# Kernel optimization log

Hardware: AMD Instinct MI355X
Metric: run time of the kernel (lower is better)

Reference implementation:

```python
import jax, jax.numpy as jnp
import numpy as np

C = 256
G = 32  # GroupNorm groups
EPS = 1e-6


def setup_inputs() -> dict:
    key = jax.random.key(0)
    ks = jax.random.split(key, 11)
    B, H, W = 4, 64, 64
    scale = 0.02
    return {
        "x": jax.random.normal(ks[0], (B, C, H, W), dtype=jnp.float32),
        "gn_scale": jnp.ones((C,), jnp.float32),
        "gn_bias": jnp.zeros((C,), jnp.float32),
        "wq": jax.random.normal(ks[1], (C, C), jnp.float32) * scale,
        "bq": jnp.zeros((C,), jnp.float32),
        "wk": jax.random.normal(ks[2], (C, C), jnp.float32) * scale,
        "bk": jnp.zeros((C,), jnp.float32),
        "wv": jax.random.normal(ks[3], (C, C), jnp.float32) * scale,
        "bv": jnp.zeros((C,), jnp.float32),
        "wp": jax.random.normal(ks[4], (C, C), jnp.float32) * scale,
        "bp": jnp.zeros((C,), jnp.float32),
    }


def _group_norm(x, scale, bias):
    b, c, h, w = x.shape
    xr = x.reshape(b, G, c // G, h, w)
    mu = jnp.mean(xr, axis=(2, 3, 4), keepdims=True)
    var = jnp.var(xr, axis=(2, 3, 4), keepdims=True)
    xn = ((xr - mu) * jax.lax.rsqrt(var + EPS)).reshape(b, c, h, w)
    return xn * scale[None, :, None, None] + bias[None, :, None, None]


def _conv1x1(x, w, bch):
    # 1x1 conv == channel-mixing matmul; w is (out_ch, in_ch)
    return jnp.einsum('bchw,dc->bdhw', x, w) + bch[None, :, None, None]


def reference(x, gn_scale, gn_bias, wq, bq, wk, bk, wv, bv, wp, bp):
    b, c, h, w = x.shape
    hn = _group_norm(x, gn_scale, gn_bias)
    q = _conv1x1(hn, wq, bq).reshape(b, c, h * w)  # (b,c,N)
    k = _conv1x1(hn, wk, bk).reshape(b, c, h * w)
    v = _conv1x1(hn, wv, bv).reshape(b, c, h * w)
    # attn[b,i,j] = softmax_j( q_i . k_j / sqrt(c) )
    attn = jax.nn.softmax(jnp.einsum('bci,bcj->bij', q, k) * (c ** -0.5), axis=-1)
    A = jnp.einsum('bcj,bij->bci', v, attn).reshape(b, c, h, w)
    return x + _conv1x1(A, wp, bp)
```

## Files before the change

kernel.cpp:

```cpp
#include <hip/hip_runtime.h>
#include <stdint.h>

#define Bn 4
#define Cn 256
#define Gn 32
#define Nn 4096
#define CGn 8

typedef unsigned short u16;
typedef __attribute__((ext_vector_type(8))) short short8;
typedef __attribute__((ext_vector_type(4))) short short4v;
typedef __attribute__((ext_vector_type(4))) float f32x4;
typedef __attribute__((ext_vector_type(16))) float f32x16;

__device__ __forceinline__ u16 f2bf(float x) {
  uint32_t u = __float_as_uint(x);
  u += 0x7fffu + ((u >> 16) & 1u);
  return (u16)(u >> 16);
}
__device__ __forceinline__ float b2f(u16 v) {
  return __uint_as_float(((uint32_t)v) << 16);
}

__device__ __forceinline__ void gl_lds16(const void* g, void* l) {
  __builtin_amdgcn_global_load_lds(
      (__attribute__((address_space(1))) void*)(uintptr_t)g,
      (__attribute__((address_space(3))) void*)(uintptr_t)l, 16, 0, 0);
}

__device__ __forceinline__ int sw512(int row, int cb) { return row * 512 + ((cb ^ (row & 7)) * 16); }

__global__ void k_cs(const float* __restrict__ wq, const float* __restrict__ wk,
                     const float* __restrict__ wv, const float* __restrict__ wp,
                     const float* __restrict__ bq, const float* __restrict__ bk,
                     const float* __restrict__ bv, const float* __restrict__ x,
                     u16* __restrict__ wqkv, u16* __restrict__ wpb,
                     float* __restrict__ bqkv, float* __restrict__ stats) {
  if (blockIdx.x < 256) {
    const float s = 0.09016844005556021f;
    int i = blockIdx.x * 256 + threadIdx.x;
    wqkv[i]          = f2bf(wq[i] * s);
    wqkv[i + 65536]  = f2bf(wk[i]);
    wqkv[i + 131072] = f2bf(wv[i]);
    wpb[i]           = f2bf(wp[i]);
    if (i < 256) { bqkv[i] = bq[i] * s; bqkv[i + 256] = bk[i]; bqkv[i + 512] = bv[i]; }
  } else {
    int blk = blockIdx.x - 256;
    int grp = blk >> 2, part = blk & 3;
    const float4* base = (const float4*)(x + (size_t)grp * (CGn * Nn) + part * 8192);
    float s = 0.f, s2 = 0.f;
    for (int i = threadIdx.x; i < 2048; i += 256) {
      float4 v = base[i];
      s  += v.x + v.y + v.z + v.w;
      s2 += v.x * v.x + v.y * v.y + v.z * v.z + v.w * v.w;
    }
#pragma unroll
    for (int m = 1; m < 64; m <<= 1) { s += __shfl_xor(s, m, 64); s2 += __shfl_xor(s2, m, 64); }
    __shared__ float ps[4], ps2[4];
    int w = threadIdx.x >> 6;
    if ((threadIdx.x & 63) == 0) { ps[w] = s; ps2[w] = s2; }
    __syncthreads();
    if (threadIdx.x == 0) {
      stats[grp * 8 + part * 2]     = ps[0] + ps[1] + ps[2] + ps[3];
      stats[grp * 8 + part * 2 + 1] = ps2[0] + ps2[1] + ps2[2] + ps2[3];
    }
  }
}

__global__ void k_apply(const float* __restrict__ x, const float* __restrict__ stats,
                        const float* __restrict__ gsc, const float* __restrict__ gbi,
                        u16* __restrict__ hnT) {
  __shared__ __align__(16) char smem[32768];
  __shared__ float smu[Gn], srs[Gn];
  int n0 = blockIdx.x * 64;
  int b = blockIdx.y;
  int tid = threadIdx.x;
  if (tid < Gn) {
    float S = 0.f, S2 = 0.f;
#pragma unroll
    for (int p = 0; p < 4; ++p) {
      S  += stats[(b * Gn + tid) * 8 + p * 2];
      S2 += stats[(b * Gn + tid) * 8 + p * 2 + 1];
    }
    const float inv = 1.f / (CGn * Nn);
    float mu = S * inv;
    float var = S2 * inv - mu * mu;
    smu[tid] = mu;
    srs[tid] = rsqrtf(var + 1e-6f);
  }
  __syncthreads();
  int nl = (tid & 15) * 4;
  int cbase = tid >> 4;
  for (int pass = 0; pass < 16; ++pass) {
    int c = pass * 16 + cbase;
    float4 v = *(const float4*)(x + (size_t)b * Cn * Nn + (size_t)c * Nn + n0 + nl);
    int g = c >> 3;
    float sc = gsc[c] * srs[g];
    float bi = gbi[c] - smu[g] * sc;
    float vals[4] = {v.x, v.y, v.z, v.w};
#pragma unroll
    for (int i = 0; i < 4; ++i) {
      int row = nl + i;
      int off = row * 512 + ((((c >> 3) + row) & 31) * 16) + (c & 7) * 2;
      *(u16*)(smem + off) = f2bf(vals[i] * sc + bi);
    }
  }
  __syncthreads();
#pragma unroll
  for (int p = 0; p < 8; ++p) {
    int idx = p * 256 + tid;
    int row = idx >> 5, pc = idx & 31;
    int gc = (pc - row) & 31;
    short8 v8 = *(const short8*)(smem + row * 512 + pc * 16);
    *(short8*)(hnT + ((size_t)b * Nn + n0 + row) * Cn + gc * 8) = v8;
  }
}

__global__ __launch_bounds__(256, 2)
void k_qkv(const u16* __restrict__ wqkv, const float* __restrict__ bqkv,
           const u16* __restrict__ hnT, u16* __restrict__ qT, u16* __restrict__ kT,
           u16* __restrict__ vv) {
  __shared__ __align__(16) char smem[65536];
  const int tid = threadIdx.x, lane = tid & 63, w = tid >> 6;
  const int quad = (lane >> 4) & 3, low = lane & 15;
  const int d0 = blockIdx.y * 64, b = blockIdx.z;
  const int n_base = blockIdx.x * 256;
  const int which = d0 >> 8;
  const int dl0 = d0 & 255;
  const u16* hb = hnT + (size_t)b * Nn * Cn;
  const int scol = lane & 31;

#define QKV_STAGE(bsel, nt)                                                     \
  {                                                                             \
    _Pragma("unroll") for (int s = 0; s < 8; ++s) {                             \
      int r = w * 16 + s * 2 + (lane >> 5);                                     \
      int gc = (scol - r) & 31;                                                 \
      gl_lds16(hb + (size_t)(n_base + (nt) * 64 + r) * Cn + gc * 8,             \
               smem + (bsel) * 32768 + (w * 16 + s * 2) * 512);                 \
    }                                                                           \
  }

  QKV_STAGE(0, 0);
  short8 af[8];
  {
    const u16* wrow = wqkv + (size_t)(d0 + w * 16 + low) * Cn + quad * 8;
#pragma unroll
    for (int kk = 0; kk < 8; ++kk) af[kk] = *(const short8*)(wrow + kk * 32);
  }
  float bias[4];
#pragma unroll
  for (int r = 0; r < 4; ++r) bias[r] = bqkv[d0 + w * 16 + quad * 4 + r];

  for (int nt = 0; nt < 4; ++nt) {
    if (nt < 3) {
      QKV_STAGE((nt + 1) & 1, nt + 1);
      asm volatile("s_waitcnt vmcnt(10)" ::: "memory");
    } else {
      asm volatile("s_waitcnt vmcnt(0)" ::: "memory");
    }
    asm volatile("s_barrier" ::: "memory");
    char* buf = smem + (nt & 1) * 32768;
    f32x4 acc[4] = {{0.f,0.f,0.f,0.f},{0.f,0.f,0.f,0.f},{0.f,0.f,0.f,0.f},{0.f,0.f,0.f,0.f}};
#pragma unroll
    for (int kk = 0; kk < 8; ++kk)
#pragma unroll
      for (int t = 0; t < 4; ++t) {
        int row = t * 16 + low;
        short8 bf = *(const short8*)(buf + row * 512 + (((kk * 4 + quad) + row) & 31) * 16);
        acc[t] = __builtin_amdgcn_mfma_f32_16x16x32_bf16(af[kk], bf, acc[t], 0, 0, 0);
      }
    asm volatile("s_barrier" ::: "memory");
    char* Q = buf + w * 8192;
    if (which == 2) {
#pragma unroll
      for (int t = 0; t < 4; ++t)
#pragma unroll
        for (int rp = 0; rp < 2; ++rp) {
          uint32_t wv2;
          float f0 = acc[t][2 * rp] + bias[2 * rp];
          float f1 = acc[t][2 * rp + 1] + bias[2 * rp + 1];
          asm("v_cvt_pk_bf16_f32 %0, %1, %2" : "=v"(wv2) : "v"(f0), "v"(f1));
          *(u16*)(Q + (quad * 4 + 2 * rp) * 144 + t * 32 + low * 2) = (u16)wv2;
          *(u16*)(Q + (quad * 4 + 2 * rp + 1) * 144 + t * 32 + low * 2) = (u16)(wv2 >> 16);
        }
#pragma unroll
      for (int s = 0; s < 2; ++s) {
        int slot = s * 64 + lane;
        int row = slot >> 3, ch = slot & 7;
        short8 v8 = *(const short8*)(Q + row * 144 + ch * 16);
        *(short8*)(vv + (size_t)b * Cn * Nn + (size_t)(dl0 + w * 16 + row) * Nn +
                   n_base + nt * 64 + ch * 8) = v8;
      }
    } else {
#pragma unroll
      for (int t = 0; t < 4; ++t) {
        union { uint32_t u[2]; short4v s; } pk;
        float f0 = acc[t][0] + bias[0], f1 = acc[t][1] + bias[1];
        float f2 = acc[t][2] + bias[2], f3 = acc[t][3] + bias[3];
        asm("v_cvt_pk_bf16_f32 %0, %1, %2" : "=v"(pk.u[0]) : "v"(f0), "v"(f1));
        asm("v_cvt_pk_bf16_f32 %0, %1, %2" : "=v"(pk.u[1]) : "v"(f2), "v"(f3));
        *(short4v*)(Q + (t * 16 + low) * 48 + quad * 8) = pk.s;
      }
      u16* dst = (which == 0 ? qT : kT) + (size_t)b * Nn * Cn;
#pragma unroll
      for (int s = 0; s < 2; ++s) {
        int slot = s * 64 + lane;
        int row = slot >> 1, half = slot & 1;
        short8 v8 = *(const short8*)(Q + row * 48 + half * 16);
        *(short8*)(dst + (size_t)(n_base + nt * 64 + row) * Cn + dl0 + w * 16 + half * 8) = v8;
      }
    }
  }
#undef QKV_STAGE
}

__device__ __forceinline__ void flash_stage(char* smem, int bsel, const u16* kTb,
                                            const u16* vb, int j0, int w, int lo,
                                            int kr, int vr, int vp) {
  char* ksb = smem + bsel * 32768;
  char* vsb = ksb + 16384;
#pragma unroll
  for (int s = 0; s < 4; ++s) {
    int j = kr + s * 2;
    int gc = (lo - j) & 31;
    gl_lds16(kTb + (size_t)(j0 + j) * Cn + gc * 8, ksb + (w * 8 + s * 2) * 512);
  }
#pragma unroll
  for (int s = 0; s < 4; ++s) {
    int c = vr + s * 16;
    int gc = (vp - c - (c >> 2)) & 3;
    gl_lds16(vb + (size_t)c * Nn + j0 + gc * 8, vsb + (w * 64 + s * 16) * 64);
  }
}

__global__ __launch_bounds__(256, 2)
void k_flash(const u16* __restrict__ qT, const u16* __restrict__ kT,
             const u16* __restrict__ vv, u16* __restrict__ Op0,
             u16* __restrict__ Op1, u16* __restrict__ Op2, u16* __restrict__ Op3,
             float* __restrict__ lrow) {
  __shared__ __align__(16) char smem[65536];
  const int tid = threadIdx.x, lane = tid & 63, w = tid >> 6;
  const int lo = lane & 31, hi = lane >> 5;
  const int i0 = blockIdx.x * 128;
  const int b = blockIdx.y, jh = blockIdx.z;
  const u16* qTb = qT + (size_t)b * Nn * Cn;
  const u16* kTb = kT + (size_t)b * Nn * Cn;
  const u16* vb  = vv + (size_t)b * Cn * Nn;
  const int u7 = lo + hi;
  const int u9 = lo + hi + (lo >> 2);
  const int kr = w * 8 + hi;
  const int vr = w * 64 + (lane >> 2);
  const int vp = lane & 3;

  flash_stage(smem, 0, kTb, vb, jh * 1024, w, lo, kr, vr, vp);

  short8 qf[16];
  {
    const u16* qrow = qTb + (size_t)(i0 + w * 32 + lo) * Cn + hi * 8;
#pragma unroll
    for (int ks = 0; ks < 16; ++ks) qf[ks] = *(const short8*)(qrow + ks * 16);
  }
  f32x16 Oa[8];
#pragma unroll
  for (int ct = 0; ct < 8; ++ct)
#pragma unroll
    for (int e = 0; e < 16; ++e) Oa[ct][e] = 0.f;
  float l_ = 0.f;

  for (int jt = 0; jt < 32; ++jt) {
    if (jt < 31) {
      flash_stage(smem, (jt + 1) & 1, kTb, vb, jh * 1024 + (jt + 1) * 32, w, lo, kr, vr, vp);
      asm volatile("s_waitcnt vmcnt(8)" ::: "memory");
    } else {
      asm volatile("s_waitcnt vmcnt(0)" ::: "memory");
    }
    asm volatile("s_barrier" ::: "memory");
    const char* ksb = smem + (jt & 1) * 32768;
    const char* vsb = ksb + 16384;

    f32x16 S0;
#pragma unroll
    for (int e = 0; e < 16; ++e) S0[e] = 0.f;
    __builtin_amdgcn_s_setprio(1);
#pragma unroll
    for (int ks = 0; ks < 16; ++ks) {
      int ch = (ks * 2 + u7) & 31;
      short8 a0 = *(const short8*)(ksb + lo * 512 + ch * 16);
      S0 = __builtin_amdgcn_mfma_f32_32x32x16_bf16(a0, qf[ks], S0, 0, 0, 0);
    }
    __builtin_amdgcn_s_setprio(0);
    uint32_t Pp[8];
#pragma unroll
    for (int g = 0; g < 8; ++g) {
      float p0 = __builtin_amdgcn_exp2f(S0[2 * g]);
      float p1 = __builtin_amdgcn_exp2f(S0[2 * g + 1]);
      l_ += p0 + p1;
      asm("v_cvt_pk_bf16_f32 %0, %1, %2" : "=v"(Pp[g]) : "v"(p0), "v"(p1));
    }
#pragma unroll
    for (int kst = 0; kst < 2; ++kst) {
      uint32_t x0 = Pp[4 * kst], x1 = Pp[4 * kst + 1];
      uint32_t y0 = Pp[4 * kst + 2], y1 = Pp[4 * kst + 3];
      asm("v_permlane32_swap_b32 %0, %1" : "+v"(x0), "+v"(y0));
      asm("v_permlane32_swap_b32 %0, %1" : "+v"(x1), "+v"(y1));
      union { uint32_t u[4]; short8 s8; } pu;
      pu.u[0] = x0;
      pu.u[1] = x1;
      pu.u[2] = y0;
      pu.u[3] = y1;
      int ch = (kst * 2 + u9) & 3;
      __builtin_amdgcn_s_setprio(1);
#pragma unroll
      for (int ct = 0; ct < 8; ++ct) {
        short8 vf = *(const short8*)(vsb + (ct * 32 + lo) * 64 + ch * 16);
        Oa[ct] = __builtin_amdgcn_mfma_f32_32x32x16_bf16(vf, pu.s8, Oa[ct], 0, 0, 0);
      }
      __builtin_amdgcn_s_setprio(0);
    }
    asm volatile("s_barrier" ::: "memory");
  }

  l_ += __shfl_xor(l_, 32, 64);
  if (hi == 0)
    lrow[(size_t)jh * (Bn * Nn) + (size_t)b * Nn + i0 + w * 32 + lo] = l_;
  float invl = __builtin_amdgcn_rcpf(l_);
  __syncthreads();
#pragma unroll
  for (int ct = 0; ct < 8; ++ct)
#pragma unroll
    for (int g = 0; g < 4; ++g) {
      union { uint32_t u[2]; short4v s; } pk;
      float f0 = Oa[ct][g * 4 + 0] * invl, f1 = Oa[ct][g * 4 + 1] * invl;
      float f2 = Oa[ct][g * 4 + 2] * invl, f3 = Oa[ct][g * 4 + 3] * invl;
      asm("v_cvt_pk_bf16_f32 %0, %1, %2" : "=v"(pk.u[0]) : "v"(f0), "v"(f1));
      asm("v_cvt_pk_bf16_f32 %0, %1, %2" : "=v"(pk.u[1]) : "v"(f2), "v"(f3));
      int chv = (ct * 4 + g + lo) & 31;
      *(short4v*)(smem + w * 16384 + lo * 512 + chv * 16 + hi * 8) = pk.s;
    }
  __syncthreads();
  u16* Opj = (jh == 0) ? Op0 : (jh == 1) ? Op1 : (jh == 2) ? Op2 : Op3;
  u16* Ob = Opj + ((size_t)b * Nn + i0 + w * 32) * (size_t)Cn;
#pragma unroll
  for (int s = 0; s < 16; ++s) {
    int rr = s * 2 + hi;
    short8 v8 = *(const short8*)(smem + w * 16384 + rr * 512 + lo * 16);
    int gc = (lo - rr) & 31;
    *(short8*)(Ob + (size_t)rr * Cn + gc * 8) = v8;
  }
}

__global__ void k_comb(const u16* __restrict__ O0, const u16* __restrict__ O1,
                       const u16* __restrict__ O2, const u16* __restrict__ O3,
                       const float* __restrict__ lrow, u16* __restrict__ OT) {
  int gid = blockIdx.x * 256 + threadIdx.x;
  int row = gid >> 6;
  int c4 = (gid & 63) << 2;
  float L = lrow[row] + lrow[Bn * Nn + row] + lrow[2 * Bn * Nn + row] + lrow[3 * Bn * Nn + row];
  float inv = __builtin_amdgcn_rcpf(L);
  size_t base = (size_t)row * Cn + c4;
  short4v a0 = *(const short4v*)(O0 + base);
  short4v a1 = *(const short4v*)(O1 + base);
  short4v a2 = *(const short4v*)(O2 + base);
  short4v a3 = *(const short4v*)(O3 + base);
  short4v o;
#pragma unroll
  for (int i = 0; i < 4; ++i)
    o[i] = (short)f2bf((b2f((u16)a0[i]) + b2f((u16)a1[i]) + b2f((u16)a2[i]) + b2f((u16)a3[i])) * inv);
  *(short4v*)(OT + base) = o;
}

__global__ __launch_bounds__(256, 2)
void k_proj(const u16* __restrict__ wpb, const float* __restrict__ bp,
            const u16* __restrict__ OT, const float* __restrict__ x,
            float* __restrict__ out) {
  __shared__ __align__(16) char smem[65536];
  int tid = threadIdx.x, lane = tid & 63, w = tid >> 6, quad = lane >> 4, low = lane & 15;
  int n0 = blockIdx.x * 64, d0 = blockIdx.y * 64, b = blockIdx.z;
  {
    int r0 = w * 16;
#pragma unroll
    for (int s = 0; s < 8; ++s) {
      int rs = r0 + s * 2;
      int r = rs + (lane >> 5);
      int cb = (lane & 31) ^ (r & 7);
      gl_lds16(wpb + (size_t)(d0 + r) * Cn + cb * 8, smem + rs * 512);
      gl_lds16(OT + ((size_t)b * Nn + n0 + r) * Cn + cb * 8, smem + 32768 + rs * 512);
    }
  }
  asm volatile("s_waitcnt vmcnt(0)" ::: "memory");
  __syncthreads();
  f32x4 acc[4] = {{0.f,0.f,0.f,0.f},{0.f,0.f,0.f,0.f},{0.f,0.f,0.f,0.f},{0.f,0.f,0.f,0.f}};
#pragma unroll
  for (int kk = 0; kk < 8; ++kk) {
    short8 af = *(const short8*)(smem + sw512(w * 16 + low, kk * 4 + quad));
#pragma unroll
    for (int t = 0; t < 4; ++t) {
      short8 bf = *(const short8*)(smem + 32768 + sw512(t * 16 + low, kk * 4 + quad));
      acc[t] = __builtin_amdgcn_mfma_f32_16x16x32_bf16(af, bf, acc[t], 0, 0, 0);
    }
  }
  int dloc = d0 + w * 16 + quad * 4;
#pragma unroll
  for (int t = 0; t < 4; ++t)
#pragma unroll
    for (int r = 0; r < 4; ++r) {
      size_t idx = (size_t)b * Cn * Nn + (size_t)(dloc + r) * Nn + n0 + t * 16 + low;
      out[idx] = x[idx] + acc[t][r] + bp[dloc + r];
    }
}

extern "C" void kernel_launch(void* const* d_in, const int* in_sizes, int n_in,
                              void* d_out, int out_size, void* d_ws, size_t ws_size,
                              hipStream_t stream) {
  const float* x   = (const float*)d_in[0];
  const float* gsc = (const float*)d_in[1];
  const float* gbi = (const float*)d_in[2];
  const float* wq  = (const float*)d_in[3];
  const float* bq  = (const float*)d_in[4];
  const float* wk  = (const float*)d_in[5];
  const float* bk  = (const float*)d_in[6];
  const float* wv  = (const float*)d_in[7];
  const float* bv  = (const float*)d_in[8];
  const float* wp  = (const float*)d_in[9];
  const float* bp  = (const float*)d_in[10];
  float* out = (float*)d_out;

  char* ws = (char*)d_ws;
  u16*   wqkv  = (u16*)(ws + 0);
  u16*   wpb   = (u16*)(ws + 393216);
  float* bqkv  = (float*)(ws + 524288);
  float* stats = (float*)(ws + 527360);
  float* lrow  = (float*)(ws + 532480);
  u16*   hnT   = (u16*)(ws + 1048576);
  u16*   qT    = (u16*)(ws + 9437184);
  u16*   kT    = (u16*)(ws + 17825792);
  u16*   vv    = (u16*)(ws + 26214400);
  u16*   Op1   = (u16*)(ws + 34603008);
  u16*   Op2   = (u16*)(ws + 42991616);
  u16*   Op3   = (u16*)(ws + 51380224);

  k_cs<<<768, 256, 0, stream>>>(wq, wk, wv, wp, bq, bk, bv, x, wqkv, wpb, bqkv, stats);
  k_apply<<<dim3(64, 4), 256, 0, stream>>>(x, stats, gsc, gbi, hnT);
  k_qkv<<<dim3(16, 12, 4), 256, 0, stream>>>(wqkv, bqkv, hnT, qT, kT, vv);
  k_flash<<<dim3(32, 4, 4), 256, 0, stream>>>(qT, kT, vv, hnT , Op1, Op2, Op3, lrow);
  k_comb<<<4096, 256, 0, stream>>>(hnT, Op1, Op2, Op3, lrow, qT );
  k_proj<<<dim3(64, 4, 4), 256, 0, stream>>>(wpb, bp, qT , x, out);
}
```

Baseline: 194.9 us.

## Fuse split-KV combine into projection kernel and split QK accumulator chain

```diff
diff --git a/kernel.cpp b/kernel.cpp
--- a/kernel.cpp
+++ b/kernel.cpp
@@ -278,22 +278,25 @@
     const char* ksb = smem + (jt & 1) * 32768;
     const char* vsb = ksb + 16384;
 
-    f32x16 S0;
-#pragma unroll
-    for (int e = 0; e < 16; ++e) S0[e] = 0.f;
+    f32x16 S0, S1;
+#pragma unroll
+    for (int e = 0; e < 16; ++e) { S0[e] = 0.f; S1[e] = 0.f; }
     __builtin_amdgcn_s_setprio(1);
 #pragma unroll
-    for (int ks = 0; ks < 16; ++ks) {
-      int ch = (ks * 2 + u7) & 31;
-      short8 a0 = *(const short8*)(ksb + lo * 512 + ch * 16);
+    for (int ks = 0; ks < 16; ks += 2) {
+      int ch0 = (ks * 2 + u7) & 31;
+      int ch1 = (ks * 2 + 2 + u7) & 31;
+      short8 a0 = *(const short8*)(ksb + lo * 512 + ch0 * 16);
+      short8 a1 = *(const short8*)(ksb + lo * 512 + ch1 * 16);
       S0 = __builtin_amdgcn_mfma_f32_32x32x16_bf16(a0, qf[ks], S0, 0, 0, 0);
+      S1 = __builtin_amdgcn_mfma_f32_32x32x16_bf16(a1, qf[ks + 1], S1, 0, 0, 0);
     }
     __builtin_amdgcn_s_setprio(0);
     uint32_t Pp[8];
 #pragma unroll
     for (int g = 0; g < 8; ++g) {
-      float p0 = __builtin_amdgcn_exp2f(S0[2 * g]);
-      float p1 = __builtin_amdgcn_exp2f(S0[2 * g + 1]);
+      float p0 = __builtin_amdgcn_exp2f(S0[2 * g] + S1[2 * g]);
+      float p1 = __builtin_amdgcn_exp2f(S0[2 * g + 1] + S1[2 * g + 1]);
       l_ += p0 + p1;
       asm("v_cvt_pk_bf16_f32 %0, %1, %2" : "=v"(Pp[g]) : "v"(p0), "v"(p1));
     }
@@ -349,30 +352,12 @@
   }
 }
 
-__global__ void k_comb(const u16* __restrict__ O0, const u16* __restrict__ O1,
-                       const u16* __restrict__ O2, const u16* __restrict__ O3,
-                       const float* __restrict__ lrow, u16* __restrict__ OT) {
-  int gid = blockIdx.x * 256 + threadIdx.x;
-  int row = gid >> 6;
-  int c4 = (gid & 63) << 2;
-  float L = lrow[row] + lrow[Bn * Nn + row] + lrow[2 * Bn * Nn + row] + lrow[3 * Bn * Nn + row];
-  float inv = __builtin_amdgcn_rcpf(L);
-  size_t base = (size_t)row * Cn + c4;
-  short4v a0 = *(const short4v*)(O0 + base);
-  short4v a1 = *(const short4v*)(O1 + base);
-  short4v a2 = *(const short4v*)(O2 + base);
-  short4v a3 = *(const short4v*)(O3 + base);
-  short4v o;
-#pragma unroll
-  for (int i = 0; i < 4; ++i)
-    o[i] = (short)f2bf((b2f((u16)a0[i]) + b2f((u16)a1[i]) + b2f((u16)a2[i]) + b2f((u16)a3[i])) * inv);
-  *(short4v*)(OT + base) = o;
-}
-
 __global__ __launch_bounds__(256, 2)
 void k_proj(const u16* __restrict__ wpb, const float* __restrict__ bp,
-            const u16* __restrict__ OT, const float* __restrict__ x,
-            float* __restrict__ out) {
+            const u16* __restrict__ O0, const u16* __restrict__ O1,
+            const u16* __restrict__ O2, const u16* __restrict__ O3,
+            const float* __restrict__ lrow,
+            const float* __restrict__ x, float* __restrict__ out) {
   __shared__ __align__(16) char smem[65536];
   int tid = threadIdx.x, lane = tid & 63, w = tid >> 6, quad = lane >> 4, low = lane & 15;
   int n0 = blockIdx.x * 64, d0 = blockIdx.y * 64, b = blockIdx.z;
@@ -384,8 +369,28 @@
       int r = rs + (lane >> 5);
       int cb = (lane & 31) ^ (r & 7);
       gl_lds16(wpb + (size_t)(d0 + r) * Cn + cb * 8, smem + rs * 512);
-      gl_lds16(OT + ((size_t)b * Nn + n0 + r) * Cn + cb * 8, smem + 32768 + rs * 512);
-    }
+    }
+  }
+#pragma unroll 4
+  for (int p = 0; p < 8; ++p) {
+    int slot = p * 256 + tid;
+    int row = slot >> 5, pc = slot & 31;
+    int gcb = pc ^ (row & 7);
+    size_t gbase = ((size_t)b * Nn + n0 + row) * Cn + gcb * 8;
+    short8 a0 = *(const short8*)(O0 + gbase);
+    short8 a1 = *(const short8*)(O1 + gbase);
+    short8 a2 = *(const short8*)(O2 + gbase);
+    short8 a3 = *(const short8*)(O3 + gbase);
+    int rrow = b * Nn + n0 + row;
+    float L = lrow[rrow] + lrow[Bn * Nn + rrow] + lrow[2 * Bn * Nn + rrow] +
+              lrow[3 * Bn * Nn + rrow];
+    float inv = __builtin_amdgcn_rcpf(L);
+    short8 o;
+#pragma unroll
+    for (int i = 0; i < 8; ++i)
+      o[i] = (short)f2bf((b2f((u16)a0[i]) + b2f((u16)a1[i]) + b2f((u16)a2[i]) +
+                          b2f((u16)a3[i])) * inv);
+    *(short8*)(smem + 32768 + row * 512 + pc * 16) = o;
   }
   asm volatile("s_waitcnt vmcnt(0)" ::: "memory");
   __syncthreads();
@@ -443,6 +448,5 @@
   k_apply<<<dim3(64, 4), 256, 0, stream>>>(x, stats, gsc, gbi, hnT);
   k_qkv<<<dim3(16, 12, 4), 256, 0, stream>>>(wqkv, bqkv, hnT, qT, kT, vv);
   k_flash<<<dim3(32, 4, 4), 256, 0, stream>>>(qT, kT, vv, hnT , Op1, Op2, Op3, lrow);
-  k_comb<<<4096, 256, 0, stream>>>(hnT, Op1, Op2, Op3, lrow, qT );
-  k_proj<<<dim3(64, 4, 4), 256, 0, stream>>>(wpb, bp, qT , x, out);
-}
+  k_proj<<<dim3(64, 4, 4), 256, 0, stream>>>(wpb, bp, hnT , Op1, Op2, Op3, lrow, x, out);
+}
```

Result: slower. 210.3 us (+7.9%).
